# Kernel tuning notes

Hardware: AMD Instinct MI355X
Metric: run time of the kernel (lower is better)

Reference implementation:

```python
import jax, jax.numpy as jnp
import numpy as np

NUM_HEADS = 16
KERNEL_SIZE = 13  # odd, neighborhood size nh = 6


def setup_inputs() -> dict:
    key = jax.random.key(0)
    ks = jax.random.split(key, 6)
    B, L, C = 4, 4096, 512
    return {
        "x": jax.random.normal(ks[0], (B, L, C), dtype=jnp.float32),
        "qkv_w": jax.random.normal(ks[1], (3 * C, C), dtype=jnp.float32) * (C ** -0.5),
        "qkv_b": jax.random.normal(ks[2], (3 * C,), dtype=jnp.float32) * 0.02,
        "rpb": jax.random.normal(ks[3], (NUM_HEADS, 2 * KERNEL_SIZE - 1), dtype=jnp.float32) * 0.02,
        "proj_w": jax.random.normal(ks[4], (C, C), dtype=jnp.float32) * (C ** -0.5),
        "proj_b": jax.random.normal(ks[5], (C,), dtype=jnp.float32) * 0.02,
    }


def reference(x, qkv_w, qkv_b, rpb, proj_w, proj_b):
    B, L, C = x.shape
    H, K = NUM_HEADS, KERNEL_SIZE
    Dh = C // H
    scale = Dh ** -0.5
    nh = K // 2

    # qkv projection (torch Linear: x @ W.T + b)
    qkv = (x @ qkv_w.T + qkv_b).reshape(B, L, 3, H, Dh)
    qkv = jnp.transpose(qkv, (2, 0, 3, 1, 4))  # (3, B, H, L, Dh)
    q, k, v = qkv[0] * scale, qkv[1], qkv[2]

    # neighborhood indices: window of K keys, shifted (not clipped) at borders
    pos = jnp.arange(L)
    start = jnp.clip(pos - nh, 0, L - K)            # (L,)
    idx = start[:, None] + jnp.arange(K)[None, :]   # (L, K) key positions
    # relative-position-bias index: (key_pos - query_pos) + (K-1), in [0, 2K-2]
    bias_idx = idx - pos[:, None] + (K - 1)         # (L, K)

    k_g = k[:, :, idx, :]                           # (B, H, L, K, Dh)
    attn = jnp.einsum('bhld,bhlkd->bhlk', q, k_g)   # (B, H, L, K)
    attn = attn + rpb[:, bias_idx][None]            # add (H, L, K) bias
    attn = jax.nn.softmax(attn, axis=-1)

    v_g = v[:, :, idx, :]                           # (B, H, L, K, Dh)
    out = jnp.einsum('bhlk,bhlkd->bhld', attn, v_g)  # (B, H, L, Dh)
    out = jnp.transpose(out, (0, 2, 1, 3)).reshape(B, L, C)
    return out @ proj_w.T + proj_b
```

## Files before the change

### kernel.cpp

```cpp
#include <hip/hip_runtime.h>
#include <hip/hip_bf16.h>

#define BATCH   4
#define LSEQ    4096
#define CCH     512
#define HNUM    16
#define DH      32
#define KSZ     13
#define NHALF   6
#define M_TOT   16384
#define N_QKV   1536
#define KDIM    512
#define BK      64

typedef __attribute__((ext_vector_type(8))) short  short8;
typedef __attribute__((ext_vector_type(4))) short  short4_t;
typedef __attribute__((ext_vector_type(4))) float  float4_t;

__device__ __forceinline__ unsigned short f32_to_bf16(float f) {
    union { float f; unsigned int u; } un; un.f = f;
    unsigned int u = un.u;
    u += 0x7FFFu + ((u >> 16) & 1u);
    return (unsigned short)(u >> 16);
}
__device__ __forceinline__ float bf16_to_f32(unsigned short h) {
    union { unsigned int u; float f; } un; un.u = ((unsigned int)h) << 16;
    return un.f;
}

__device__ __forceinline__ void gload_lds16(const unsigned short* g, unsigned short* l) {
    __builtin_amdgcn_global_load_lds(
        (const __attribute__((address_space(1))) unsigned int*)g,
        (__attribute__((address_space(3))) unsigned int*)l,
        16, 0, 0);
}

__global__ void cvt_all(const float4_t* __restrict__ xin,  short4_t* __restrict__ xo,  int nx,
                        const float4_t* __restrict__ w1in, short4_t* __restrict__ w1o, int n1,
                        const float4_t* __restrict__ w2in, short4_t* __restrict__ w2o, int n2) {
    int i = blockIdx.x * blockDim.x + threadIdx.x;
    int stride = gridDim.x * blockDim.x;
    int ntot = nx + n1 + n2;
    for (; i < ntot; i += stride) {
        const float4_t* src; short4_t* dst; int j;
        if (i < nx)            { src = xin;  dst = xo;  j = i; }
        else if (i < nx + n1)  { src = w1in; dst = w1o; j = i - nx; }
        else                   { src = w2in; dst = w2o; j = i - nx - n1; }
        float4_t v = src[j];
        short4_t h;
        h.x = (short)f32_to_bf16(v.x);
        h.y = (short)f32_to_bf16(v.y);
        h.z = (short)f32_to_bf16(v.z);
        h.w = (short)f32_to_bf16(v.w);
        dst[j] = h;
    }
}

__global__ __launch_bounds__(256) void gemm_qkv(
    const unsigned short* __restrict__ Xb,
    const unsigned short* __restrict__ W,
    const float* __restrict__ bias,
    unsigned short* __restrict__ qkvout)
{
    extern __shared__ __align__(16) unsigned short lds[];
    const int tid  = threadIdx.x;
    const int wv   = tid >> 6, ln = tid & 63;
    const int m0   = blockIdx.x * 128;
    const int n0   = blockIdx.y * 128;
    const int wm   = (wv >> 1) * 64;
    const int wn   = (wv & 1) * 64;
    const int lr   = ln & 15;
    const int lg   = ln >> 4;
    const int rgrp = ln >> 3;
    const int csw  = ((ln & 7) ^ rgrp) * 8;

    float4_t acc[4][4];
    #pragma unroll
    for (int m = 0; m < 4; ++m)
        #pragma unroll
        for (int n = 0; n < 4; ++n)
            acc[m][n] = (float4_t){0.f, 0.f, 0.f, 0.f};

    #define STAGE(k0_, abuf_, bbuf_) do {                                     \
        _Pragma("unroll")                                                     \
        for (int it_ = 0; it_ < 4; ++it_) {                                   \
            int ch_  = it_ * 4 + wv;                                          \
            int row_ = ch_ * 8 + rgrp;                                        \
            gload_lds16(Xb + (size_t)(m0 + row_) * KDIM + (k0_) + csw,        \
                        (abuf_) + ch_ * 8 * BK);                              \
            gload_lds16(W  + (size_t)(n0 + row_) * KDIM + (k0_) + csw,        \
                        (bbuf_) + ch_ * 8 * BK);                              \
        }                                                                     \
    } while (0)

    unsigned short* Ac = lds;           unsigned short* Bc = lds + 8192;
    unsigned short* An = lds + 16384;   unsigned short* Bn = lds + 24576;

    STAGE(0, Ac, Bc);

    for (int t = 0; t < 8; ++t) {
        if (t < 7) {
            STAGE((t + 1) * BK, An, Bn);
            asm volatile("s_waitcnt vmcnt(8)" ::: "memory");
        } else {
            asm volatile("s_waitcnt vmcnt(0)" ::: "memory");
        }
        __builtin_amdgcn_s_barrier();

        short8 af[2][4], bfr[2][4];
        #pragma unroll
        for (int kk = 0; kk < 2; ++kk) {
            #pragma unroll
            for (int m = 0; m < 4; ++m) {
                int row = wm + m * 16 + lr;
                int c   = (kk * 4 + lg) ^ (row & 7);
                af[kk][m] = *reinterpret_cast<const short8*>(&Ac[row * BK + c * 8]);
            }
            #pragma unroll
            for (int n = 0; n < 4; ++n) {
                int row = wn + n * 16 + lr;
                int c   = (kk * 4 + lg) ^ (row & 7);
                bfr[kk][n] = *reinterpret_cast<const short8*>(&Bc[row * BK + c * 8]);
            }
        }
        #pragma unroll
        for (int kk = 0; kk < 2; ++kk)
            #pragma unroll
            for (int m = 0; m < 4; ++m)
                #pragma unroll
                for (int n = 0; n < 4; ++n)
                    acc[m][n] = __builtin_amdgcn_mfma_f32_16x16x32_bf16(
                        af[kk][m], bfr[kk][n], acc[m][n], 0, 0, 0);

        if (t < 7) __builtin_amdgcn_s_barrier();
        unsigned short* tA = Ac; Ac = An; An = tA;
        unsigned short* tB = Bc; Bc = Bn; Bn = tB;
    }
    #undef STAGE

    const float qscale = 0.17677669529663687f;
    #pragma unroll
    for (int m = 0; m < 4; ++m) {
        #pragma unroll
        for (int n = 0; n < 4; ++n) {
            int gn    = n0 + wn + n * 16 + lr;
            int which = gn >> 9;
            int hh    = (gn >> 5) & 15;
            int dd    = gn & 31;
            float bsv = bias[gn];
            #pragma unroll
            for (int r = 0; r < 4; ++r) {
                int gm = m0 + wm + m * 16 + lg * 4 + r;
                float v = acc[m][n][r] + bsv;
                if (which == 0) v *= qscale;
                int b_ = gm >> 12, l = gm & 4095;
                size_t off = (((size_t)which * BATCH + b_) * HNUM + hh) *
                                 ((size_t)LSEQ * DH) + (size_t)l * DH + dd;
                qkvout[off] = f32_to_bf16(v);
            }
        }
    }
}

__global__ __launch_bounds__(256) void natten_fwd(
    const unsigned short* __restrict__ qkv,
    const float* __restrict__ rpb,
    unsigned short* __restrict__ ctx)
{
    #define NRP 280
    __shared__ __align__(16) unsigned short vt[DH * NRP];
    __shared__ __align__(16) unsigned short pl[4 * 16 * 32];
    __shared__ float rpb_s[25];

    const int t    = threadIdx.x;
    const int wv   = t >> 6, ln = t & 63;
    const int lblk = blockIdx.x & 15;
    const int bh   = blockIdx.x >> 4;
    const int hh   = bh & 15, b_ = bh >> 4;
    const int l0b  = lblk * 256;
    const int r0   = l0b - 6;

    const size_t plane = (size_t)LSEQ * DH;
    const size_t qbase = (((size_t)0 * BATCH + b_) * HNUM + hh) * plane;
    const size_t kbase = (((size_t)1 * BATCH + b_) * HNUM + hh) * plane;
    const size_t vbase = (((size_t)2 * BATCH + b_) * HNUM + hh) * plane;

    for (int kr = t; kr < 276; kr += 256) {
        int ka = min(max(r0 + kr, 0), LSEQ - 1);
        #pragma unroll
        for (int cq = 0; cq < 4; ++cq) {
            short8 v = *reinterpret_cast<const short8*>(&qkv[vbase + (size_t)ka * DH + cq * 8]);
            #pragma unroll
            for (int e = 0; e < 8; ++e)
                vt[(cq * 8 + e) * NRP + kr] = (unsigned short)v[e];
        }
    }
    if (t < 25) rpb_s[t] = rpb[hh * 25 + t];
    __syncthreads();

    const int g = ln >> 4;
    const int c = ln & 15;

    #pragma unroll
    for (int qi = 0; qi < 4; ++qi) {
        const int l0 = l0b + wv * 64 + qi * 16;
        const int k0 = l0 - 6;

        short8 qf = *reinterpret_cast<const short8*>(
            &qkv[qbase + (size_t)(l0 + c) * DH + g * 8]);
        int key0c = min(max(k0 + c, 0), LSEQ - 1);
        int key1c = min(max(k0 + 16 + c, 0), LSEQ - 1);
        short8 kf0 = *reinterpret_cast<const short8*>(
            &qkv[kbase + (size_t)key0c * DH + g * 8]);
        short8 kf1 = *reinterpret_cast<const short8*>(
            &qkv[kbase + (size_t)key1c * DH + g * 8]);
        float4_t s0 = (float4_t){0.f, 0.f, 0.f, 0.f};
        float4_t s1 = (float4_t){0.f, 0.f, 0.f, 0.f};
        s0 = __builtin_amdgcn_mfma_f32_16x16x32_bf16(qf, kf0, s0, 0, 0, 0);
        s1 = __builtin_amdgcn_mfma_f32_16x16x32_bf16(qf, kf1, s1, 0, 0, 0);

        const int ka0 = k0 + c;
        const int ka1 = k0 + 16 + c;
        #pragma unroll
        for (int r = 0; r < 4; ++r) {
            int tok = l0 + g * 4 + r;
            int st  = min(max(tok - NHALF, 0), LSEQ - KSZ);
            bool v0 = (ka0 >= st) && (ka0 < st + KSZ);
            bool v1 = (ka1 >= st) && (ka1 < st + KSZ);
            float b0 = rpb_s[min(max(ka0 - tok + 12, 0), 24)];
            float b1 = rpb_s[min(max(ka1 - tok + 12, 0), 24)];
            float x0 = v0 ? s0[r] + b0 : -1e30f;
            float x1 = v1 ? s1[r] + b1 : -1e30f;
            float m = fmaxf(x0, x1);
            #pragma unroll
            for (int d = 1; d < 16; d <<= 1) m = fmaxf(m, __shfl_xor(m, d));
            float e0 = v0 ? __expf(x0 - m) : 0.f;
            float e1 = v1 ? __expf(x1 - m) : 0.f;
            float s = e0 + e1;
            #pragma unroll
            for (int d = 1; d < 16; d <<= 1) s += __shfl_xor(s, d);
            float inv = 1.f / s;
            pl[wv * 512 + (g * 4 + r) * 32 + c]      = f32_to_bf16(e0 * inv);
            pl[wv * 512 + (g * 4 + r) * 32 + 16 + c] = f32_to_bf16(e1 * inv);
        }

        short8 pa = *reinterpret_cast<const short8*>(
            &pl[wv * 512 + c * 32 + g * 8]);
        int k0rel = l0 - l0b;
        short8 vb0 = *reinterpret_cast<const short8*>(
            &vt[c * NRP + k0rel + g * 8]);
        short8 vb1 = *reinterpret_cast<const short8*>(
            &vt[(16 + c) * NRP + k0rel + g * 8]);
        float4_t o0 = (float4_t){0.f, 0.f, 0.f, 0.f};
        float4_t o1 = (float4_t){0.f, 0.f, 0.f, 0.f};
        o0 = __builtin_amdgcn_mfma_f32_16x16x32_bf16(pa, vb0, o0, 0, 0, 0);
        o1 = __builtin_amdgcn_mfma_f32_16x16x32_bf16(pa, vb1, o1, 0, 0, 0);

        #pragma unroll
        for (int r = 0; r < 4; ++r) {
            size_t ob = ((size_t)(b_ * LSEQ + l0 + g * 4 + r)) * CCH + hh * DH;
            ctx[ob + c]      = f32_to_bf16(o0[r]);
            ctx[ob + 16 + c] = f32_to_bf16(o1[r]);
        }
    }
    #undef NRP
}

__global__ __launch_bounds__(256) void gemm_proj(
    const unsigned short* __restrict__ Xb,
    const unsigned short* __restrict__ W,
    const float* __restrict__ bias,
    float* __restrict__ out)
{
    extern __shared__ __align__(16) unsigned short lds[];
    const int tid  = threadIdx.x;
    const int wv   = tid >> 6, ln = tid & 63;
    const int m0   = blockIdx.x * 128;
    const int n0   = blockIdx.y * 128;
    const int wm   = (wv >> 1) * 64;
    const int wn   = (wv & 1) * 64;
    const int lr   = ln & 15;
    const int lg   = ln >> 4;
    const int rgrp = ln >> 3;
    const int csw  = ((ln & 7) ^ rgrp) * 8;

    float4_t acc[4][4];
    #pragma unroll
    for (int m = 0; m < 4; ++m)
        #pragma unroll
        for (int n = 0; n < 4; ++n)
            acc[m][n] = (float4_t){0.f, 0.f, 0.f, 0.f};

    #define STAGEP(k0_, abuf_, bbuf_) do {                                    \
        _Pragma("unroll")                                                     \
        for (int it_ = 0; it_ < 4; ++it_) {                                   \
            int ch_  = it_ * 4 + wv;                                          \
            int row_ = ch_ * 8 + rgrp;                                        \
            gload_lds16(Xb + (size_t)(m0 + row_) * KDIM + (k0_) + csw,        \
                        (abuf_) + ch_ * 8 * BK);                              \
            gload_lds16(W  + (size_t)(n0 + row_) * KDIM + (k0_) + csw,        \
                        (bbuf_) + ch_ * 8 * BK);                              \
        }                                                                     \
    } while (0)

    unsigned short* Ac = lds;           unsigned short* Bc = lds + 8192;
    unsigned short* An = lds + 16384;   unsigned short* Bn = lds + 24576;

    STAGEP(0, Ac, Bc);

    for (int t = 0; t < 8; ++t) {
        if (t < 7) {
            STAGEP((t + 1) * BK, An, Bn);
            asm volatile("s_waitcnt vmcnt(8)" ::: "memory");
        } else {
            asm volatile("s_waitcnt vmcnt(0)" ::: "memory");
        }
        __builtin_amdgcn_s_barrier();

        short8 af[2][4], bfr[2][4];
        #pragma unroll
        for (int kk = 0; kk < 2; ++kk) {
            #pragma unroll
            for (int m = 0; m < 4; ++m) {
                int row = wm + m * 16 + lr;
                int c   = (kk * 4 + lg) ^ (row & 7);
                af[kk][m] = *reinterpret_cast<const short8*>(&Ac[row * BK + c * 8]);
            }
            #pragma unroll
            for (int n = 0; n < 4; ++n) {
                int row = wn + n * 16 + lr;
                int c   = (kk * 4 + lg) ^ (row & 7);
                bfr[kk][n] = *reinterpret_cast<const short8*>(&Bc[row * BK + c * 8]);
            }
        }
        #pragma unroll
        for (int kk = 0; kk < 2; ++kk)
            #pragma unroll
            for (int m = 0; m < 4; ++m)
                #pragma unroll
                for (int n = 0; n < 4; ++n)
                    acc[m][n] = __builtin_amdgcn_mfma_f32_16x16x32_bf16(
                        af[kk][m], bfr[kk][n], acc[m][n], 0, 0, 0);

        if (t < 7) __builtin_amdgcn_s_barrier();
        unsigned short* tA = Ac; Ac = An; An = tA;
        unsigned short* tB = Bc; Bc = Bn; Bn = tB;
    }
    #undef STAGEP

    #pragma unroll
    for (int m = 0; m < 4; ++m) {
        #pragma unroll
        for (int n = 0; n < 4; ++n) {
            int gn = n0 + wn + n * 16 + lr;
            float bsv = bias[gn];
            #pragma unroll
            for (int r = 0; r < 4; ++r) {
                int gm = m0 + wm + m * 16 + lg * 4 + r;
                out[(size_t)gm * CCH + gn] = acc[m][n][r] + bsv;
            }
        }
    }
}

extern "C" void kernel_launch(void* const* d_in, const int* in_sizes, int n_in,
                              void* d_out, int out_size, void* d_ws, size_t ws_size,
                              hipStream_t stream) {
    const float* x      = (const float*)d_in[0];
    const float* qkv_w  = (const float*)d_in[1];
    const float* qkv_b  = (const float*)d_in[2];
    const float* rpb    = (const float*)d_in[3];
    const float* proj_w = (const float*)d_in[4];
    const float* proj_b = (const float*)d_in[5];
    float* out = (float*)d_out;
    char* ws = (char*)d_ws;

    unsigned short* qkv = (unsigned short*)(ws);
    unsigned short* xb  = (unsigned short*)(ws + 50331648);
    unsigned short* ctx = (unsigned short*)(ws + 50331648);
    unsigned short* wq  = (unsigned short*)(ws + 67108864);
    unsigned short* wp  = (unsigned short*)(ws + 68681728);

    cvt_all<<<2048, 256, 0, stream>>>(
        (const float4_t*)x,      (short4_t*)xb, M_TOT * KDIM / 4,
        (const float4_t*)qkv_w,  (short4_t*)wq, 786432 / 4,
        (const float4_t*)proj_w, (short4_t*)wp, 262144 / 4);

    dim3 g1(M_TOT / 128, N_QKV / 128);
    gemm_qkv<<<g1, 256, 65536, stream>>>(xb, wq, qkv_b, qkv);

    natten_fwd<<<BATCH * HNUM * (LSEQ / 256), 256, 0, stream>>>(qkv, rpb, ctx);

    dim3 g2(M_TOT / 128, CCH / 128);
    gemm_proj<<<g2, 256, 65536, stream>>>(ctx, wp, proj_b, out);
}
```

Measured before the change: 76.79 us.

## Enlarge QKV GEMM tile to 256x256 with 8 waves and interleaved staged pipeline

The QKV projection GEMM moves from 128x128 tiles with 4 waves to 256x256 tiles with 8 waves and 128KB of LDS. The main loop is restructured into quarter-tile MFMA blocks, with global-to-LDS loads for the next k-step split into halves and interleaved between them, plus s_setprio around the MFMAs. The aim is more data reuse per tile and better overlap of loads with matrix math. In exchange it launches fewer blocks (384) with one block per CU, which may leave CUs underused, and it adds many barriers.

Result: slower. 85.31 us (+11.1%).

```diff
diff --git a/kernel.cpp b/kernel.cpp
--- a/kernel.cpp
+++ b/kernel.cpp
@@ -56,7 +56,7 @@
     }
 }
 
-__global__ __launch_bounds__(256) void gemm_qkv(
+__global__ __launch_bounds__(512, 1) void gemm_qkv(
     const unsigned short* __restrict__ Xb,
     const unsigned short* __restrict__ W,
     const float* __restrict__ bias,
@@ -65,93 +65,153 @@
     extern __shared__ __align__(16) unsigned short lds[];
     const int tid  = threadIdx.x;
     const int wv   = tid >> 6, ln = tid & 63;
-    const int m0   = blockIdx.x * 128;
-    const int n0   = blockIdx.y * 128;
-    const int wm   = (wv >> 1) * 64;
-    const int wn   = (wv & 1) * 64;
+    const int m0   = blockIdx.x * 256;
+    const int n0   = blockIdx.y * 256;
+    const int wm   = (wv >> 2) * 128;
+    const int wn   = (wv & 3) * 64;
     const int lr   = ln & 15;
     const int lg   = ln >> 4;
     const int rgrp = ln >> 3;
     const int csw  = ((ln & 7) ^ rgrp) * 8;
 
-    float4_t acc[4][4];
+    float4_t acc[8][4];
     #pragma unroll
-    for (int m = 0; m < 4; ++m)
+    for (int m = 0; m < 8; ++m)
         #pragma unroll
         for (int n = 0; n < 4; ++n)
             acc[m][n] = (float4_t){0.f, 0.f, 0.f, 0.f};
 
-    #define STAGE(k0_, abuf_, bbuf_) do {                                     \
+    #define STAGE_HALF(t_, isB_, h_) do {                                     \
+        const unsigned short* src_ = (isB_) ? W : Xb;                         \
+        const int gb_ = (isB_) ? n0 : m0;                                     \
+        unsigned short* dst_ = lds + ((isB_) ? 32768 : 0) + ((t_) & 1) * 16384;\
+        const int k0_ = (t_) * BK;                                            \
         _Pragma("unroll")                                                     \
-        for (int it_ = 0; it_ < 4; ++it_) {                                   \
-            int ch_  = it_ * 4 + wv;                                          \
-            int row_ = ch_ * 8 + rgrp;                                        \
-            gload_lds16(Xb + (size_t)(m0 + row_) * KDIM + (k0_) + csw,        \
-                        (abuf_) + ch_ * 8 * BK);                              \
-            gload_lds16(W  + (size_t)(n0 + row_) * KDIM + (k0_) + csw,        \
-                        (bbuf_) + ch_ * 8 * BK);                              \
+        for (int j_ = 0; j_ < 2; ++j_) {                                      \
+            int rb_ = (h_) * 128 + wv * 16 + j_ * 8;                          \
+            gload_lds16(src_ + (size_t)(gb_ + rb_ + rgrp) * KDIM + k0_ + csw, \
+                        dst_ + rb_ * 64);                                     \
         }                                                                     \
     } while (0)
 
-    unsigned short* Ac = lds;           unsigned short* Bc = lds + 8192;
-    unsigned short* An = lds + 16384;   unsigned short* Bn = lds + 24576;
-
-    STAGE(0, Ac, Bc);
-
-    for (int t = 0; t < 8; ++t) {
-        if (t < 7) {
-            STAGE((t + 1) * BK, An, Bn);
-            asm volatile("s_waitcnt vmcnt(8)" ::: "memory");
+    short8 af[2][4], b0f[2][2], b1f[2][2];
+
+    #define READ_A(t_, QM_) do {                                              \
+        const unsigned short* Ab_ = lds + ((t_) & 1) * 16384;                 \
+        _Pragma("unroll")                                                     \
+        for (int kk_ = 0; kk_ < 2; ++kk_)                                     \
+            _Pragma("unroll")                                                 \
+            for (int m_ = 0; m_ < 4; ++m_) {                                  \
+                int row_ = wm + (QM_) * 64 + m_ * 16 + lr;                    \
+                af[kk_][m_] = *reinterpret_cast<const short8*>(               \
+                    &Ab_[row_ * 64 + ((kk_ * 4 + lg) ^ (row_ & 7)) * 8]);     \
+            }                                                                 \
+    } while (0)
+
+    #define READ_B(t_, QN_, BF_) do {                                         \
+        const unsigned short* Bb_ = lds + 32768 + ((t_) & 1) * 16384;         \
+        _Pragma("unroll")                                                     \
+        for (int kk_ = 0; kk_ < 2; ++kk_)                                     \
+            _Pragma("unroll")                                                 \
+            for (int n_ = 0; n_ < 2; ++n_) {                                  \
+                int row_ = wn + (QN_) * 32 + n_ * 16 + lr;                    \
+                BF_[kk_][n_] = *reinterpret_cast<const short8*>(              \
+                    &Bb_[row_ * 64 + ((kk_ * 4 + lg) ^ (row_ & 7)) * 8]);     \
+            }                                                                 \
+    } while (0)
+
+    #define MFMA16(QM_, QN_, BF_) do {                                        \
+        __builtin_amdgcn_s_setprio(1);                                        \
+        _Pragma("unroll")                                                     \
+        for (int kk_ = 0; kk_ < 2; ++kk_)                                     \
+            _Pragma("unroll")                                                 \
+            for (int m_ = 0; m_ < 4; ++m_)                                    \
+                _Pragma("unroll")                                             \
+                for (int n_ = 0; n_ < 2; ++n_)                                \
+                    acc[(QM_) * 4 + m_][(QN_) * 2 + n_] =                     \
+                        __builtin_amdgcn_mfma_f32_16x16x32_bf16(              \
+                            af[kk_][m_], BF_[kk_][n_],                        \
+                            acc[(QM_) * 4 + m_][(QN_) * 2 + n_], 0, 0, 0);    \
+        __builtin_amdgcn_s_setprio(0);                                        \
+    } while (0)
+
+    #define BAR()  __builtin_amdgcn_s_barrier()
+    #define SBAR() __builtin_amdgcn_sched_barrier(0)
+
+    STAGE_HALF(0, 0, 0); STAGE_HALF(0, 0, 1);
+    STAGE_HALF(0, 1, 0); STAGE_HALF(0, 1, 1);
+
+    for (int i = 0; i < 4; ++i) {
+        const int tE = 2 * i, tO = 2 * i + 1, tN = 2 * i + 2;
+
+        STAGE_HALF(tO, 0, 0);
+        asm volatile("s_waitcnt vmcnt(2)" ::: "memory");
+        BAR(); SBAR();
+        READ_A(tE, 0); READ_B(tE, 0, b0f);
+        BAR();
+        MFMA16(0, 0, b0f);
+        BAR();
+        STAGE_HALF(tO, 0, 1);
+        READ_B(tE, 1, b1f);
+        BAR();
+        MFMA16(0, 1, b1f);
+        BAR();
+        STAGE_HALF(tO, 1, 0);
+        READ_A(tE, 1);
+        BAR();
+        MFMA16(1, 1, b1f);
+        BAR();
+        STAGE_HALF(tO, 1, 1);
+        BAR();
+        MFMA16(1, 0, b0f);
+        BAR();
+        if (tN < 8) {
+            STAGE_HALF(tN, 0, 0);
+            asm volatile("s_waitcnt vmcnt(2)" ::: "memory");
         } else {
             asm volatile("s_waitcnt vmcnt(0)" ::: "memory");
         }
-        __builtin_amdgcn_s_barrier();
-
-        short8 af[2][4], bfr[2][4];
-        #pragma unroll
-        for (int kk = 0; kk < 2; ++kk) {
-            #pragma unroll
-            for (int m = 0; m < 4; ++m) {
-                int row = wm + m * 16 + lr;
-                int c   = (kk * 4 + lg) ^ (row & 7);
-                af[kk][m] = *reinterpret_cast<const short8*>(&Ac[row * BK + c * 8]);
-            }
-            #pragma unroll
-            for (int n = 0; n < 4; ++n) {
-                int row = wn + n * 16 + lr;
-                int c   = (kk * 4 + lg) ^ (row & 7);
-                bfr[kk][n] = *reinterpret_cast<const short8*>(&Bc[row * BK + c * 8]);
-            }
-        }
-        #pragma unroll
-        for (int kk = 0; kk < 2; ++kk)
-            #pragma unroll
-            for (int m = 0; m < 4; ++m)
-                #pragma unroll
-                for (int n = 0; n < 4; ++n)
-                    acc[m][n] = __builtin_amdgcn_mfma_f32_16x16x32_bf16(
-                        af[kk][m], bfr[kk][n], acc[m][n], 0, 0, 0);
-
-        if (t < 7) __builtin_amdgcn_s_barrier();
-        unsigned short* tA = Ac; Ac = An; An = tA;
-        unsigned short* tB = Bc; Bc = Bn; Bn = tB;
-    }
-    #undef STAGE
+        BAR(); SBAR();
+        READ_A(tO, 0); READ_B(tO, 0, b0f);
+        BAR();
+        MFMA16(0, 0, b0f);
+        BAR();
+        if (tN < 8) STAGE_HALF(tN, 0, 1);
+        READ_B(tO, 1, b1f);
+        BAR();
+        MFMA16(0, 1, b1f);
+        BAR();
+        if (tN < 8) STAGE_HALF(tN, 1, 0);
+        READ_A(tO, 1);
+        BAR();
+        MFMA16(1, 1, b1f);
+        BAR();
+        if (tN < 8) STAGE_HALF(tN, 1, 1);
+        BAR();
+        MFMA16(1, 0, b0f);
+        BAR();
+    }
+    #undef STAGE_HALF
+    #undef READ_A
+    #undef READ_B
+    #undef MFMA16
+    #undef BAR
+    #undef SBAR
 
     const float qscale = 0.17677669529663687f;
     #pragma unroll
-    for (int m = 0; m < 4; ++m) {
-        #pragma unroll
-        for (int n = 0; n < 4; ++n) {
-            int gn    = n0 + wn + n * 16 + lr;
+    for (int mf = 0; mf < 8; ++mf) {
+        #pragma unroll
+        for (int nf = 0; nf < 4; ++nf) {
+            int gn    = n0 + wn + nf * 16 + lr;
             int which = gn >> 9;
             int hh    = (gn >> 5) & 15;
             int dd    = gn & 31;
             float bsv = bias[gn];
             #pragma unroll
             for (int r = 0; r < 4; ++r) {
-                int gm = m0 + wm + m * 16 + lg * 4 + r;
-                float v = acc[m][n][r] + bsv;
+                int gm = m0 + wm + mf * 16 + lg * 4 + r;
+                float v = acc[mf][nf][r] + bsv;
                 if (which == 0) v *= qscale;
                 int b_ = gm >> 12, l = gm & 4095;
                 size_t off = (((size_t)which * BATCH + b_) * HNUM + hh) *
@@ -386,8 +446,8 @@
         (const float4_t*)qkv_w,  (short4_t*)wq, 786432 / 4,
         (const float4_t*)proj_w, (short4_t*)wp, 262144 / 4);
 
-    dim3 g1(M_TOT / 128, N_QKV / 128);
-    gemm_qkv<<<g1, 256, 65536, stream>>>(xb, wq, qkv_b, qkv);
+    dim3 g1(M_TOT / 256, N_QKV / 256);
+    gemm_qkv<<<g1, 512, 131072, stream>>>(xb, wq, qkv_b, qkv);
 
     natten_fwd<<<BATCH * HNUM * (LSEQ / 256), 256, 0, stream>>>(qkv, rpb, ctx);
 
```
